# Performance work log

Hardware: AMD Instinct MI355X
Metric: run time of the kernel (lower is better)

## Reference

```python
import jax, jax.numpy as jnp
import numpy as np

EMBED = 1024
HEADS = 16
HDIM = 64
OUT = 1024
SCALE = HDIM ** (-0.5)


def setup_inputs() -> dict:
    key = jax.random.key(0)
    ks = jax.random.split(key, 12)
    B, L = 4, 1024
    k = jax.random.normal(ks[0], (B, L, EMBED), dtype=jnp.float32)
    q = jax.random.normal(ks[1], (B, L, EMBED), dtype=jnp.float32)
    v = jax.random.normal(ks[2], (B, L, EMBED), dtype=jnp.float32)
    # Linear params stored as [in, out]; scaled like torch default init
    lim = EMBED ** (-0.5)
    Wq = jax.random.uniform(ks[3], (EMBED, HEADS * HDIM), jnp.float32, -lim, lim)
    bq = jax.random.uniform(ks[4], (HEADS * HDIM,), jnp.float32, -lim, lim)
    Wk = jax.random.uniform(ks[5], (EMBED, HEADS * HDIM), jnp.float32, -lim, lim)
    Wv = jax.random.uniform(ks[6], (EMBED, HEADS * HDIM), jnp.float32, -lim, lim)
    limp = (HEADS * HDIM) ** (-0.5)
    Wp = jax.random.uniform(ks[7], (HEADS * HDIM, OUT), jnp.float32, -limp, limp)
    bp = jax.random.uniform(ks[8], (OUT,), jnp.float32, -limp, limp)
    attn_w = jax.random.uniform(ks[9], (2 * HDIM,), jnp.float32, -SCALE, SCALE)
    gamma = jnp.ones((OUT,), jnp.float32)
    beta = jnp.zeros((OUT,), jnp.float32)
    return {"k": k, "q": q, "v": v, "Wq": Wq, "bq": bq, "Wk": Wk, "Wv": Wv,
            "Wp": Wp, "bp": bp, "attn_w": attn_w, "gamma": gamma, "beta": beta}


def reference(k, q, v, Wq, bq, Wk, Wv, Wp, bp, attn_w, gamma, beta):
    B, Lq = q.shape[0], q.shape[1]
    Lk = k.shape[1]
    # QKV projections -> (b, len, heads, hdim)
    qh = (q @ Wq + bq).reshape(B, Lq, HEADS, HDIM)
    kh = (k @ Wk).reshape(B, Lk, HEADS, HDIM)
    vh = (v @ Wv).reshape(B, Lk, HEADS, HDIM)
    # mlp score: tanh(cat(q_i, k_j) . w) == tanh(q_i.w1 + k_j.w2); avoids
    # materializing the (b, q, k, n, 2d) padded tensor from the original.
    w1, w2 = attn_w[:HDIM], attn_w[HDIM:]
    sq = jnp.einsum('bind,d->bin', qh, w1)  # (b, q_len, heads)
    sk = jnp.einsum('bjnd,d->bjn', kh, w2)  # (b, k_len, heads)
    attn = jnp.tanh(sq[:, :, None, :] + sk[:, None, :, :])  # (b, i, j, n)
    attn = jax.nn.softmax(attn, axis=2)  # softmax over k_len (dim=2)
    out = jnp.einsum('bijn,bjnd->bind', attn, vh).reshape(B, Lq, HEADS * HDIM)
    out = out @ Wp + bp
    # LayerNorm eps=1e-6 (dropout is identity at p=0)
    mean = jnp.mean(out, axis=-1, keepdims=True)
    var = jnp.var(out, axis=-1, keepdims=True)
    out = (out - mean) / jnp.sqrt(var + 1e-6) * gamma + beta
    return out
```

## Files before the change

### kernel.cpp

```cpp
#include <hip/hip_runtime.h>
#include <math.h>

#define HEADS 16
#define HDIM  64
#define SEQ   1024
#define ROWS  4096
#define EMB   1024
#define MN    16

typedef _Float16 f16;
typedef __attribute__((ext_vector_type(4))) _Float16 f16x4;
typedef __attribute__((ext_vector_type(8))) _Float16 f16x8;
typedef __attribute__((ext_vector_type(4))) float f32x4;

__global__ __launch_bounds__(256) void fold_kernel(
    const float* __restrict__ Wq, const float* __restrict__ Wk,
    const float* __restrict__ bq, const float* __restrict__ attn_w,
    float* __restrict__ uq, float* __restrict__ uk, float* __restrict__ cq)
{
  int bid = blockIdx.x;
  if (bid < 128) {
    int idx = bid*256 + threadIdx.x;
    bool isQ = idx < 16384;
    int li = isQ ? idx : idx - 16384;
    int e = li >> 4, n = li & 15;
    const float* W = isQ ? Wq : Wk;
    const float* w = isQ ? attn_w : attn_w + HDIM;
    const float* wp = &W[(size_t)e*EMB + n*HDIM];
    float s = 0.f;
    #pragma unroll 16
    for (int d = 0; d < HDIM; ++d) s = fmaf(wp[d], w[d], s);
    (isQ ? uq : uk)[li] = s;
  } else if (threadIdx.x < 16) {
    int n = threadIdx.x;
    float s = 0.f;
    for (int d = 0; d < HDIM; ++d) s = fmaf(bq[n*HDIM+d], attn_w[d], s);
    cq[n] = s;
  }
}

__global__ __launch_bounds__(256) void sqsk2_kernel(
    const float* __restrict__ q, const float* __restrict__ k,
    const float* __restrict__ uq, const float* __restrict__ uk,
    const float* __restrict__ cq, float* __restrict__ sq, float* __restrict__ sk)
{
  __shared__ float rowbuf[8][EMB];
  __shared__ float part[16][8][17];
  int bid = blockIdx.x;
  bool isQ = bid < 512;
  int row0 = (isQ ? bid : bid - 512) * 8;
  const float* X = isQ ? q : k;
  const float* U = isQ ? uq : uk;
  int tid = threadIdx.x;
  #pragma unroll
  for (int p = 0; p < 8; ++p) {
    int fi = p*256 + tid;
    int r = fi >> 8, c4 = (fi & 255) * 4;
    *reinterpret_cast<float4*>(&rowbuf[r][c4]) =
        *reinterpret_cast<const float4*>(&X[(size_t)(row0 + r)*EMB + c4]);
  }
  __syncthreads();
  int n = tid & 15, ch = tid >> 4;
  float acc[8] = {0,0,0,0,0,0,0,0};
  #pragma unroll 4
  for (int e0 = 0; e0 < 64; ++e0) {
    int e = ch*64 + e0;
    float u = U[e*16 + n];
    #pragma unroll
    for (int r = 0; r < 8; ++r) acc[r] = fmaf(rowbuf[r][e], u, acc[r]);
  }
  #pragma unroll
  for (int r = 0; r < 8; ++r) part[ch][r][n] = acc[r];
  __syncthreads();
  if (tid < 128) {
    int r = tid >> 4, nn = tid & 15;
    float t = isQ ? cq[nn] : 0.f;
    #pragma unroll
    for (int c = 0; c < 16; ++c) t += part[c][r][nn];
    (isQ ? sq : sk)[(size_t)(row0 + r)*16 + nn] = t;
  }
}

__global__ __launch_bounds__(256) void nodes_kernel(const float* __restrict__ sq,
                                                    float* __restrict__ nodes)
{
  int bn = blockIdx.x;
  int b = bn >> 4, n = bn & 15;
  int tid = threadIdx.x;
  float mn = 1e30f, mx = -1e30f;
  #pragma unroll
  for (int s = 0; s < 4; ++s) {
    float v = sq[((size_t)(b*SEQ + tid + s*256))*16 + n];
    mn = fminf(mn, v); mx = fmaxf(mx, v);
  }
  __shared__ float smn[256], smx[256];
  smn[tid] = mn; smx[tid] = mx;
  __syncthreads();
  for (int off = 128; off > 0; off >>= 1) {
    if (tid < off) { smn[tid] = fminf(smn[tid], smn[tid+off]);
                     smx[tid] = fmaxf(smx[tid], smx[tid+off]); }
    __syncthreads();
  }
  if (tid < MN) {
    float c = 0.5f*(smn[0] + smx[0]);
    float r = fmaxf(0.5f*(smx[0] - smn[0]), 1e-4f);
    nodes[bn*MN + tid] = c + r * cosf(tid * (3.14159265358979323f / (MN-1)));
  }
}

__global__ __launch_bounds__(256) void ztrans_kernel(
    const float* __restrict__ v, const float* __restrict__ Wv,
    f16* __restrict__ vTh, f16* __restrict__ WvTh)
{
  __shared__ float tile[64][65];
  const int z = blockIdx.z;
  const int r0 = blockIdx.y * 64, c0 = blockIdx.x * 64;
  const int t = threadIdx.x, rr = t >> 4, c4 = (t & 15) * 4;
  const float* src = (z < 4) ? &v[(size_t)(z*SEQ + r0)*EMB + c0]
                             : &Wv[(size_t)r0*EMB + c0];
  #pragma unroll
  for (int i = 0; i < 4; ++i) {
    int row = rr + i * 16;
    float4 w = *reinterpret_cast<const float4*>(&src[(size_t)row*EMB + c4]);
    tile[row][c4] = w.x; tile[row][c4+1] = w.y;
    tile[row][c4+2] = w.z; tile[row][c4+3] = w.w;
  }
  __syncthreads();
  #pragma unroll
  for (int i = 0; i < 4; ++i) {
    int cc = rr + i * 16;
    f16x4 hh;
    #pragma unroll
    for (int jj = 0; jj < 4; ++jj) hh[jj] = (f16)tile[c4 + jj][cc];
    size_t o = (z < 4) ? ((size_t)(z*EMB + c0 + cc))*SEQ + r0 + c4
                       : ((size_t)(c0 + cc))*EMB + r0 + c4;
    *reinterpret_cast<f16x4*>(&((z < 4) ? vTh : WvTh)[o]) = hh;
  }
}

__global__ __launch_bounds__(256) void wmat_kernel(
    const float* __restrict__ sk, const float* __restrict__ nodes,
    f16* __restrict__ wh, float* __restrict__ Wn)
{
  __shared__ float sksh[256], nodesh[MN], Wnl[MN];
  const int qd = blockIdx.x, n = blockIdx.y, b = blockIdx.z;
  const int tid = threadIdx.x;
  const int j = qd*256 + tid;
  sksh[tid] = sk[((size_t)(b*SEQ + j))*16 + n];
  if (tid < MN) { nodesh[tid] = nodes[(b*16+n)*MN + tid]; Wnl[tid] = 0.f; }
  __syncthreads();
  const float skv = sksh[tid];
  const int lane = tid & 63;
  #pragma unroll 4
  for (int m = 0; m < MN; ++m) {
    float s = nodesh[m] + skv;
    float e2 = __expf(2.f * s);
    float th = 1.f - 2.f / (e2 + 1.f);
    float w = __expf(th);
    size_t row = (size_t)(b*256 + n*MN + m);
    wh[row*1024 + j] = (f16)w;
    float ws = w;
    #pragma unroll
    for (int off = 32; off > 0; off >>= 1) ws += __shfl_xor(ws, off);
    if (lane == 0) atomicAdd(&Wnl[m], ws);
  }
  __syncthreads();
  if (tid < MN) atomicAdd(&Wn[(b*16+n)*MN + tid], Wnl[tid]);
}

__global__ __launch_bounds__(256) void gemm1_f16(
    const f16* __restrict__ Ah, const f16* __restrict__ Bh,
    f16* __restrict__ Ch)
{
  __shared__ __align__(16) char lds[16384];
  const int tid = threadIdx.x;
  const int wid = tid >> 6, lane = tid & 63;
  int flat = blockIdx.y * 16 + blockIdx.x;
  int swz = (flat & 7) * 32 + (flat >> 3);
  const int bx = swz & 15, by = swz >> 4;
  const int z = by >> 2;
  const int grow = by * 64;
  const int bcol = bx * 64;
  const int wm = wid >> 1, wn = wid & 1;
  const int asel = lane >> 4, l15 = lane & 15;
  const int K = 1024, N = 1024;
  const f16* Bz_h = Bh + (size_t)z*EMB*SEQ;

  f32x4 acc[2][2];
  #pragma unroll
  for (int i = 0; i < 2; ++i)
    #pragma unroll
    for (int jx = 0; jx < 2; ++jx)
      acc[i][jx] = (f32x4){0.f, 0.f, 0.f, 0.f};

  for (int t = 0; t < 16; ++t) {
    const int k0 = t * 64;
    __syncthreads();
    #pragma unroll
    for (int r = 0; r < 4; ++r) {
      int ci = ((r & 1) << 8) + tid;
      int row = ci >> 3, kc = ci & 7;
      int kcg = kc ^ (row & 7);
      const f16* base = (r < 2) ? Ah : Bz_h;
      size_t roff = (r < 2) ? (size_t)(grow + row) : (size_t)(bcol + row);
      const char* src = (const char*)(base + roff * K + k0 + kcg * 8);
      char* dst = lds + (r * 256 + wid * 64) * 16;
      __builtin_amdgcn_global_load_lds(
          (const __attribute__((address_space(1))) unsigned int*)src,
          (__attribute__((address_space(3))) unsigned int*)dst, 16, 0, 0);
    }
    __syncthreads();
    #pragma unroll
    for (int kk = 0; kk < 2; ++kk) {
      f16x8 afh[2], bfh[2];
      #pragma unroll
      for (int mf = 0; mf < 2; ++mf) {
        int row = wm * 32 + mf * 16 + l15;
        int kcx = (kk * 4 + asel) ^ (row & 7);
        afh[mf] = *reinterpret_cast<const f16x8*>(lds + row * 128 + kcx * 16);
      }
      #pragma unroll
      for (int nf = 0; nf < 2; ++nf) {
        int col = wn * 32 + nf * 16 + l15;
        int kcx = (kk * 4 + asel) ^ (col & 7);
        bfh[nf] = *reinterpret_cast<const f16x8*>(lds + 8192 + col * 128 + kcx * 16);
      }
      #pragma unroll
      for (int mf = 0; mf < 2; ++mf)
        #pragma unroll
        for (int nf = 0; nf < 2; ++nf)
          acc[mf][nf] = __builtin_amdgcn_mfma_f32_16x16x32_f16(afh[mf], bfh[nf], acc[mf][nf], 0, 0, 0);
    }
  }
  const int crow0 = grow + wm * 32 + asel * 4;
  const int ccol0 = bcol + wn * 32 + l15;
  #pragma unroll
  for (int nf = 0; nf < 2; ++nf)
    #pragma unroll
    for (int mf = 0; mf < 2; ++mf)
      #pragma unroll
      for (int jx = 0; jx < 4; ++jx)
        Ch[(size_t)(crow0 + mf*16 + jx) * N + ccol0 + nf*16] = (f16)acc[mf][nf][jx];
}

__global__ __launch_bounds__(256) void coeff2_kernel(
    const float* __restrict__ sq, const float* __restrict__ nodes,
    const float* __restrict__ Wn, f16* __restrict__ csh, f16* __restrict__ csl)
{
  __shared__ float nsh[16][MN], wsh[16][MN];
  const int ic = blockIdx.x, b = blockIdx.y;
  const int tid = threadIdx.x;
  {
    int nn = tid >> 4, mm = tid & 15;
    nsh[nn][mm] = nodes[(b*16+nn)*MN + mm];
    wsh[nn][mm] = Wn[(b*16+nn)*MN + mm];
  }
  __syncthreads();
  const int il = tid >> 4, n = tid & 15;
  const int i = ic*16 + il;
  float s = sq[((size_t)(b*SEQ + i))*16 + n];
  float lam[MN];
  float den = 0.f;
  int ex = -1;
  #pragma unroll
  for (int m = 0; m < MN; ++m) {
    float diff = s - nsh[n][m];
    float wb = ((m == 0) | (m == MN-1)) ? 0.5f : 1.0f;
    wb = (m & 1) ? -wb : wb;
    if (diff == 0.f) ex = m;
    lam[m] = wb / diff;
    den = fmaf(lam[m], wsh[n][m], den);
  }
  float rden = 1024.f / den;
  f16* hp = &csh[((size_t)(b*SEQ + i))*256 + n*MN];
  f16* lp = &csl[((size_t)(b*SEQ + i))*256 + n*MN];
  #pragma unroll
  for (int m8 = 0; m8 < 2; ++m8) {
    f16x8 hv, lv;
    #pragma unroll
    for (int jj = 0; jj < 8; ++jj) {
      int m = m8*8 + jj;
      float c = (ex >= 0) ? ((m == ex) ? 1024.f/wsh[n][ex] : 0.f) : lam[m]*rden;
      f16 h = (f16)c;
      hv[jj] = h; lv[jj] = (f16)(c - (float)h);
    }
    *reinterpret_cast<f16x8*>(&hp[m8*8]) = hv;
    *reinterpret_cast<f16x8*>(&lp[m8*8]) = lv;
  }
}

__global__ __launch_bounds__(256) void ghprep_kernel(
    const f16* __restrict__ Ph, const f16* __restrict__ WvTh,
    const float* __restrict__ Wp, f16* __restrict__ Hsh, f16* __restrict__ Hsl)
{
  __shared__ float Gsh[MN][64];
  const int oc = blockIdx.x, n = blockIdx.y, b = blockIdx.z;
  const int bn = b*16 + n;
  const int tid = threadIdx.x;
  const int w = tid >> 6, lane = tid & 63;
  const int l15 = lane & 15, asel = lane >> 4;
  f32x4 acc = (f32x4){0.f,0.f,0.f,0.f};
  #pragma unroll 4
  for (int ks = 0; ks < 32; ++ks) {
    size_t bo = ((size_t)(n*64 + w*16 + l15))*1024 + ks*32 + asel*8;
    f16x8 bh = *reinterpret_cast<const f16x8*>(&WvTh[bo]);
    size_t ao = ((size_t)(bn*MN + l15))*1024 + ks*32 + asel*8;
    f16x8 ah = *reinterpret_cast<const f16x8*>(&Ph[ao]);
    acc = __builtin_amdgcn_mfma_f32_16x16x32_f16(ah, bh, acc, 0, 0, 0);
  }
  #pragma unroll
  for (int jx = 0; jx < 4; ++jx)
    Gsh[asel*4 + jx][w*16 + l15] = acc[jx];
  __syncthreads();
  const int o = oc*256 + tid;
  float a2[MN];
  #pragma unroll
  for (int m = 0; m < MN; ++m) a2[m] = 0.f;
  for (int d = 0; d < 64; ++d) {
    float wp = Wp[(size_t)(n*64 + d)*1024 + o];
    #pragma unroll
    for (int m = 0; m < MN; ++m) a2[m] = fmaf(wp, Gsh[m][d], a2[m]);
  }
  f16 hbuf[MN], lbuf[MN];
  #pragma unroll
  for (int m = 0; m < MN; ++m) {
    float vv = a2[m] * (1.f/1024.f);
    f16 h = (f16)vv;
    hbuf[m] = h; lbuf[m] = (f16)(vv - (float)h);
  }
  size_t base = ((size_t)(b*1024 + o))*256 + n*MN;
  #pragma unroll
  for (int m8 = 0; m8 < 2; ++m8) {
    *reinterpret_cast<f16x8*>(&Hsh[base + m8*8]) = *reinterpret_cast<f16x8*>(&hbuf[m8*8]);
    *reinterpret_cast<f16x8*>(&Hsl[base + m8*8]) = *reinterpret_cast<f16x8*>(&lbuf[m8*8]);
  }
}

__global__ __launch_bounds__(256) void gemm2_k(
    const f16* __restrict__ Ah, const f16* __restrict__ Al,
    const f16* __restrict__ Bh, const f16* __restrict__ Bl,
    const float* __restrict__ bias, float* __restrict__ Cf)
{
  __shared__ __align__(16) char lds[49152];
  const int tid = threadIdx.x;
  const int wid = tid >> 6, lane = tid & 63;
  int flat = (blockIdx.z * 8 + blockIdx.y) * 16 + blockIdx.x;
  int swz = (flat & 7) * 64 + (flat >> 3);
  const int bx = swz & 15;
  const int t2 = swz >> 4;
  const int by = t2 & 7, z = t2 >> 3;
  const int brow = by * 128;
  const int bcol = bx * 64;
  const int wm = wid >> 1, wn = wid & 1;
  const int asel = lane >> 4, l15 = lane & 15;
  const int K = 256, N = 1024, MZ = 1024;
  const f16* Az_h = Ah + (size_t)z*MZ*K;
  const f16* Az_l = Al + (size_t)z*MZ*K;
  const f16* Bz_h = Bh + (size_t)z*N*K;
  const f16* Bz_l = Bl + (size_t)z*N*K;

  f32x4 acc[4][2];
  #pragma unroll
  for (int i = 0; i < 4; ++i)
    #pragma unroll
    for (int jx = 0; jx < 2; ++jx)
      acc[i][jx] = (f32x4){0.f, 0.f, 0.f, 0.f};

  for (int t = 0; t < 4; ++t) {
    const int k0 = t * 64;
    __syncthreads();
    #pragma unroll
    for (int r = 0; r < 12; ++r) {
      const char* src;
      if (r < 8) {
        int ci = ((r & 3) << 8) + tid;
        int row = ci >> 3, kc = ci & 7;
        int kcg = kc ^ (row & 7);
        const f16* base = (r < 4) ? Az_h : Az_l;
        src = (const char*)(base + (size_t)(brow + row) * K + k0 + kcg * 8);
      } else {
        int ci = ((r & 1) << 8) + tid;
        int col = ci >> 3, kc = ci & 7;
        int kcg = kc ^ (col & 7);
        const f16* base = (r < 10) ? Bz_h : Bz_l;
        src = (const char*)(base + (size_t)(bcol + col) * K + k0 + kcg * 8);
      }
      char* dst = lds + (r * 256 + wid * 64) * 16;
      __builtin_amdgcn_global_load_lds(
          (const __attribute__((address_space(1))) unsigned int*)src,
          (__attribute__((address_space(3))) unsigned int*)dst, 16, 0, 0);
    }
    __syncthreads();
    #pragma unroll
    for (int kk = 0; kk < 2; ++kk) {
      f16x8 afh[4], afl[4], bfh[2], bfl[2];
      #pragma unroll
      for (int mf = 0; mf < 4; ++mf) {
        int row = wm * 64 + mf * 16 + l15;
        int kcx = (kk * 4 + asel) ^ (row & 7);
        int off = row * 128 + kcx * 16;
        afh[mf] = *reinterpret_cast<const f16x8*>(lds + off);
        afl[mf] = *reinterpret_cast<const f16x8*>(lds + 16384 + off);
      }
      #pragma unroll
      for (int nf = 0; nf < 2; ++nf) {
        int col = wn * 32 + nf * 16 + l15;
        int kcx = (kk * 4 + asel) ^ (col & 7);
        int off = col * 128 + kcx * 16;
        bfh[nf] = *reinterpret_cast<const f16x8*>(lds + 32768 + off);
        bfl[nf] = *reinterpret_cast<const f16x8*>(lds + 40960 + off);
      }
      #pragma unroll
      for (int mf = 0; mf < 4; ++mf)
        #pragma unroll
        for (int nf = 0; nf < 2; ++nf) {
          acc[mf][nf] = __builtin_amdgcn_mfma_f32_16x16x32_f16(afh[mf], bfh[nf], acc[mf][nf], 0, 0, 0);
          acc[mf][nf] = __builtin_amdgcn_mfma_f32_16x16x32_f16(afh[mf], bfl[nf], acc[mf][nf], 0, 0, 0);
          acc[mf][nf] = __builtin_amdgcn_mfma_f32_16x16x32_f16(afl[mf], bfh[nf], acc[mf][nf], 0, 0, 0);
        }
    }
  }
  const int crow0 = z*MZ + brow + wm * 64 + asel * 4;
  const int ccol0 = bcol + wn * 32 + l15;
  #pragma unroll
  for (int nf = 0; nf < 2; ++nf) {
    float bv = bias[ccol0 + nf * 16];
    #pragma unroll
    for (int mf = 0; mf < 4; ++mf)
      #pragma unroll
      for (int jx = 0; jx < 4; ++jx)
        Cf[(size_t)(crow0 + mf*16 + jx) * N + ccol0 + nf*16] = acc[mf][nf][jx] + bv;
  }
}

__global__ __launch_bounds__(256) void ln_kernel(
    float* __restrict__ out, const float* __restrict__ gamma,
    const float* __restrict__ beta)
{
  int row = blockIdx.x, tid = threadIdx.x;
  float4 x = *reinterpret_cast<float4*>(&out[(size_t)row*EMB + tid*4]);
  float sum = x.x + x.y + x.z + x.w;
  float ssq = x.x*x.x + x.y*x.y + x.z*x.z + x.w*x.w;
  #pragma unroll
  for (int off = 32; off > 0; off >>= 1) {
    sum += __shfl_down(sum, off);
    ssq += __shfl_down(ssq, off);
  }
  __shared__ float red[8];
  int wave = tid >> 6, lane = tid & 63;
  if (lane == 0) { red[wave] = sum; red[4+wave] = ssq; }
  __syncthreads();
  if (tid == 0) {
    float a = red[0]+red[1]+red[2]+red[3];
    float qq = red[4]+red[5]+red[6]+red[7];
    float mean = a * (1.f/EMB);
    float var  = qq * (1.f/EMB) - mean*mean;
    red[0] = mean;
    red[1] = 1.0f / sqrtf(var + 1e-6f);
  }
  __syncthreads();
  float mean = red[0], inv = red[1];
  float4 gv = *reinterpret_cast<const float4*>(&gamma[tid*4]);
  float4 bv = *reinterpret_cast<const float4*>(&beta[tid*4]);
  x.x = (x.x - mean)*inv*gv.x + bv.x;
  x.y = (x.y - mean)*inv*gv.y + bv.y;
  x.z = (x.z - mean)*inv*gv.z + bv.z;
  x.w = (x.w - mean)*inv*gv.w + bv.w;
  *reinterpret_cast<float4*>(&out[(size_t)row*EMB + tid*4]) = x;
}

extern "C" void kernel_launch(void* const* d_in, const int* in_sizes, int n_in,
                              void* d_out, int out_size, void* d_ws, size_t ws_size,
                              hipStream_t stream)
{
  const float* k   = (const float*)d_in[0];
  const float* q   = (const float*)d_in[1];
  const float* v   = (const float*)d_in[2];
  const float* Wq  = (const float*)d_in[3];
  const float* bq  = (const float*)d_in[4];
  const float* Wk  = (const float*)d_in[5];
  const float* Wv  = (const float*)d_in[6];
  const float* Wp  = (const float*)d_in[7];
  const float* bp  = (const float*)d_in[8];
  const float* aw  = (const float*)d_in[9];
  const float* gamma = (const float*)d_in[10];
  const float* beta  = (const float*)d_in[11];
  float* out = (float*)d_out;

  float* ws    = (float*)d_ws;
  float* uq    = ws;
  float* uk    = uq + 16384;
  float* cq    = uk + 16384;
  float* sq    = cq + 16;
  float* sk    = sq + 65536;
  float* nodes = sk + 65536;
  float* Wn    = nodes + 1024;
  const size_t MEG = 1048576;
  f16* f16b  = (f16*)(ws + 165904);
  f16* WvTh  = f16b;
  f16* vTh   = f16b + 1*MEG;
  f16* wh    = f16b + 5*MEG;
  f16* Ph    = f16b + 6*MEG;
  f16* csh   = f16b + 7*MEG;
  f16* csl   = f16b + 8*MEG;
  f16* Hsh   = f16b + 9*MEG;
  f16* Hsl   = f16b + 10*MEG;

  fold_kernel<<<129, 256, 0, stream>>>(Wq, Wk, bq, aw, uq, uk, cq);
  sqsk2_kernel<<<1024, 256, 0, stream>>>(q, k, uq, uk, cq, sq, sk);
  nodes_kernel<<<64, 256, 0, stream>>>(sq, nodes);
  ztrans_kernel<<<dim3(16,16,5), 256, 0, stream>>>(v, Wv, vTh, WvTh);
  hipMemsetAsync(Wn, 0, 1024*sizeof(float), stream);
  wmat_kernel<<<dim3(4,16,4), 256, 0, stream>>>(sk, nodes, wh, Wn);
  gemm1_f16<<<dim3(16,16), 256, 0, stream>>>(wh, vTh, Ph);
  coeff2_kernel<<<dim3(64,4), 256, 0, stream>>>(sq, nodes, Wn, csh, csl);
  ghprep_kernel<<<dim3(4,16,4), 256, 0, stream>>>(Ph, WvTh, Wp, Hsh, Hsl);
  gemm2_k<<<dim3(16,8,4), 256, 0, stream>>>(csh, csl, Hsh, Hsl, bp, out);
  ln_kernel<<<ROWS, 256, 0, stream>>>(out, gamma, beta);
}
```

Measured before the change: 196.1 us.

## Fuse all stages into one persistent cooperative kernel with grid syncs

```diff
diff --git a/kernel.cpp b/kernel.cpp
--- a/kernel.cpp
+++ b/kernel.cpp
@@ -1,10 +1,10 @@
 #include <hip/hip_runtime.h>
+#include <hip/hip_cooperative_groups.h>
 #include <math.h>
 
-#define HEADS 16
-#define HDIM  64
+namespace cg = cooperative_groups;
+
 #define SEQ   1024
-#define ROWS  4096
 #define EMB   1024
 #define MN    16
 
@@ -13,508 +13,479 @@
 typedef __attribute__((ext_vector_type(8))) _Float16 f16x8;
 typedef __attribute__((ext_vector_type(4))) float f32x4;
 
-__global__ __launch_bounds__(256) void fold_kernel(
-    const float* __restrict__ Wq, const float* __restrict__ Wk,
-    const float* __restrict__ bq, const float* __restrict__ attn_w,
-    float* __restrict__ uq, float* __restrict__ uk, float* __restrict__ cq)
+struct Params {
+  const float *k, *q, *v, *Wq, *bq, *Wk, *Wv, *Wp, *bp, *aw, *gamma, *beta;
+  float *out;
+  float *uq, *uk, *cq, *sq, *sk, *nodes, *Wn;
+  f16 *WvTh, *vTh, *wh, *Ph, *csh, *csl, *Hsh, *Hsl;
+  int NB;
+};
+
+__global__ __launch_bounds__(256, 4) void mega_kernel(Params P)
 {
-  int bid = blockIdx.x;
-  if (bid < 128) {
-    int idx = bid*256 + threadIdx.x;
-    bool isQ = idx < 16384;
-    int li = isQ ? idx : idx - 16384;
-    int e = li >> 4, n = li & 15;
-    const float* W = isQ ? Wq : Wk;
-    const float* w = isQ ? attn_w : attn_w + HDIM;
-    const float* wp = &W[(size_t)e*EMB + n*HDIM];
-    float s = 0.f;
-    #pragma unroll 16
-    for (int d = 0; d < HDIM; ++d) s = fmaf(wp[d], w[d], s);
-    (isQ ? uq : uk)[li] = s;
-  } else if (threadIdx.x < 16) {
-    int n = threadIdx.x;
-    float s = 0.f;
-    for (int d = 0; d < HDIM; ++d) s = fmaf(bq[n*HDIM+d], attn_w[d], s);
-    cq[n] = s;
-  }
-}
-
-__global__ __launch_bounds__(256) void sqsk2_kernel(
-    const float* __restrict__ q, const float* __restrict__ k,
-    const float* __restrict__ uq, const float* __restrict__ uk,
-    const float* __restrict__ cq, float* __restrict__ sq, float* __restrict__ sk)
-{
-  __shared__ float rowbuf[8][EMB];
-  __shared__ float part[16][8][17];
-  int bid = blockIdx.x;
-  bool isQ = bid < 512;
-  int row0 = (isQ ? bid : bid - 512) * 8;
-  const float* X = isQ ? q : k;
-  const float* U = isQ ? uq : uk;
-  int tid = threadIdx.x;
-  #pragma unroll
-  for (int p = 0; p < 8; ++p) {
-    int fi = p*256 + tid;
-    int r = fi >> 8, c4 = (fi & 255) * 4;
-    *reinterpret_cast<float4*>(&rowbuf[r][c4]) =
-        *reinterpret_cast<const float4*>(&X[(size_t)(row0 + r)*EMB + c4]);
-  }
-  __syncthreads();
-  int n = tid & 15, ch = tid >> 4;
-  float acc[8] = {0,0,0,0,0,0,0,0};
-  #pragma unroll 4
-  for (int e0 = 0; e0 < 64; ++e0) {
-    int e = ch*64 + e0;
-    float u = U[e*16 + n];
-    #pragma unroll
-    for (int r = 0; r < 8; ++r) acc[r] = fmaf(rowbuf[r][e], u, acc[r]);
-  }
-  #pragma unroll
-  for (int r = 0; r < 8; ++r) part[ch][r][n] = acc[r];
-  __syncthreads();
-  if (tid < 128) {
-    int r = tid >> 4, nn = tid & 15;
-    float t = isQ ? cq[nn] : 0.f;
-    #pragma unroll
-    for (int c = 0; c < 16; ++c) t += part[c][r][nn];
-    (isQ ? sq : sk)[(size_t)(row0 + r)*16 + nn] = t;
-  }
-}
-
-__global__ __launch_bounds__(256) void nodes_kernel(const float* __restrict__ sq,
-                                                    float* __restrict__ nodes)
-{
-  int bn = blockIdx.x;
-  int b = bn >> 4, n = bn & 15;
-  int tid = threadIdx.x;
-  float mn = 1e30f, mx = -1e30f;
-  #pragma unroll
-  for (int s = 0; s < 4; ++s) {
-    float v = sq[((size_t)(b*SEQ + tid + s*256))*16 + n];
-    mn = fminf(mn, v); mx = fmaxf(mx, v);
-  }
-  __shared__ float smn[256], smx[256];
-  smn[tid] = mn; smx[tid] = mx;
-  __syncthreads();
-  for (int off = 128; off > 0; off >>= 1) {
-    if (tid < off) { smn[tid] = fminf(smn[tid], smn[tid+off]);
-                     smx[tid] = fmaxf(smx[tid], smx[tid+off]); }
-    __syncthreads();
-  }
-  if (tid < MN) {
-    float c = 0.5f*(smn[0] + smx[0]);
-    float r = fmaxf(0.5f*(smx[0] - smn[0]), 1e-4f);
-    nodes[bn*MN + tid] = c + r * cosf(tid * (3.14159265358979323f / (MN-1)));
-  }
-}
-
-__global__ __launch_bounds__(256) void ztrans_kernel(
-    const float* __restrict__ v, const float* __restrict__ Wv,
-    f16* __restrict__ vTh, f16* __restrict__ WvTh)
-{
-  __shared__ float tile[64][65];
-  const int z = blockIdx.z;
-  const int r0 = blockIdx.y * 64, c0 = blockIdx.x * 64;
-  const int t = threadIdx.x, rr = t >> 4, c4 = (t & 15) * 4;
-  const float* src = (z < 4) ? &v[(size_t)(z*SEQ + r0)*EMB + c0]
-                             : &Wv[(size_t)r0*EMB + c0];
-  #pragma unroll
-  for (int i = 0; i < 4; ++i) {
-    int row = rr + i * 16;
-    float4 w = *reinterpret_cast<const float4*>(&src[(size_t)row*EMB + c4]);
-    tile[row][c4] = w.x; tile[row][c4+1] = w.y;
-    tile[row][c4+2] = w.z; tile[row][c4+3] = w.w;
-  }
-  __syncthreads();
-  #pragma unroll
-  for (int i = 0; i < 4; ++i) {
-    int cc = rr + i * 16;
-    f16x4 hh;
-    #pragma unroll
-    for (int jj = 0; jj < 4; ++jj) hh[jj] = (f16)tile[c4 + jj][cc];
-    size_t o = (z < 4) ? ((size_t)(z*EMB + c0 + cc))*SEQ + r0 + c4
-                       : ((size_t)(c0 + cc))*EMB + r0 + c4;
-    *reinterpret_cast<f16x4*>(&((z < 4) ? vTh : WvTh)[o]) = hh;
-  }
-}
-
-__global__ __launch_bounds__(256) void wmat_kernel(
-    const float* __restrict__ sk, const float* __restrict__ nodes,
-    f16* __restrict__ wh, float* __restrict__ Wn)
-{
-  __shared__ float sksh[256], nodesh[MN], Wnl[MN];
-  const int qd = blockIdx.x, n = blockIdx.y, b = blockIdx.z;
-  const int tid = threadIdx.x;
-  const int j = qd*256 + tid;
-  sksh[tid] = sk[((size_t)(b*SEQ + j))*16 + n];
-  if (tid < MN) { nodesh[tid] = nodes[(b*16+n)*MN + tid]; Wnl[tid] = 0.f; }
-  __syncthreads();
-  const float skv = sksh[tid];
-  const int lane = tid & 63;
-  #pragma unroll 4
-  for (int m = 0; m < MN; ++m) {
-    float s = nodesh[m] + skv;
-    float e2 = __expf(2.f * s);
-    float th = 1.f - 2.f / (e2 + 1.f);
-    float w = __expf(th);
-    size_t row = (size_t)(b*256 + n*MN + m);
-    wh[row*1024 + j] = (f16)w;
-    float ws = w;
-    #pragma unroll
-    for (int off = 32; off > 0; off >>= 1) ws += __shfl_xor(ws, off);
-    if (lane == 0) atomicAdd(&Wnl[m], ws);
-  }
-  __syncthreads();
-  if (tid < MN) atomicAdd(&Wn[(b*16+n)*MN + tid], Wnl[tid]);
-}
-
-__global__ __launch_bounds__(256) void gemm1_f16(
-    const f16* __restrict__ Ah, const f16* __restrict__ Bh,
-    f16* __restrict__ Ch)
-{
-  __shared__ __align__(16) char lds[16384];
-  const int tid = threadIdx.x;
-  const int wid = tid >> 6, lane = tid & 63;
-  int flat = blockIdx.y * 16 + blockIdx.x;
-  int swz = (flat & 7) * 32 + (flat >> 3);
-  const int bx = swz & 15, by = swz >> 4;
-  const int z = by >> 2;
-  const int grow = by * 64;
-  const int bcol = bx * 64;
-  const int wm = wid >> 1, wn = wid & 1;
-  const int asel = lane >> 4, l15 = lane & 15;
-  const int K = 1024, N = 1024;
-  const f16* Bz_h = Bh + (size_t)z*EMB*SEQ;
-
-  f32x4 acc[2][2];
-  #pragma unroll
-  for (int i = 0; i < 2; ++i)
-    #pragma unroll
-    for (int jx = 0; jx < 2; ++jx)
-      acc[i][jx] = (f32x4){0.f, 0.f, 0.f, 0.f};
-
-  for (int t = 0; t < 16; ++t) {
-    const int k0 = t * 64;
-    __syncthreads();
-    #pragma unroll
-    for (int r = 0; r < 4; ++r) {
-      int ci = ((r & 1) << 8) + tid;
-      int row = ci >> 3, kc = ci & 7;
-      int kcg = kc ^ (row & 7);
-      const f16* base = (r < 2) ? Ah : Bz_h;
-      size_t roff = (r < 2) ? (size_t)(grow + row) : (size_t)(bcol + row);
-      const char* src = (const char*)(base + roff * K + k0 + kcg * 8);
-      char* dst = lds + (r * 256 + wid * 64) * 16;
-      __builtin_amdgcn_global_load_lds(
-          (const __attribute__((address_space(1))) unsigned int*)src,
-          (__attribute__((address_space(3))) unsigned int*)dst, 16, 0, 0);
-    }
-    __syncthreads();
-    #pragma unroll
-    for (int kk = 0; kk < 2; ++kk) {
-      f16x8 afh[2], bfh[2];
-      #pragma unroll
-      for (int mf = 0; mf < 2; ++mf) {
-        int row = wm * 32 + mf * 16 + l15;
-        int kcx = (kk * 4 + asel) ^ (row & 7);
-        afh[mf] = *reinterpret_cast<const f16x8*>(lds + row * 128 + kcx * 16);
-      }
-      #pragma unroll
-      for (int nf = 0; nf < 2; ++nf) {
-        int col = wn * 32 + nf * 16 + l15;
-        int kcx = (kk * 4 + asel) ^ (col & 7);
-        bfh[nf] = *reinterpret_cast<const f16x8*>(lds + 8192 + col * 128 + kcx * 16);
-      }
-      #pragma unroll
-      for (int mf = 0; mf < 2; ++mf)
-        #pragma unroll
-        for (int nf = 0; nf < 2; ++nf)
-          acc[mf][nf] = __builtin_amdgcn_mfma_f32_16x16x32_f16(afh[mf], bfh[nf], acc[mf][nf], 0, 0, 0);
-    }
-  }
-  const int crow0 = grow + wm * 32 + asel * 4;
-  const int ccol0 = bcol + wn * 32 + l15;
-  #pragma unroll
-  for (int nf = 0; nf < 2; ++nf)
-    #pragma unroll
-    for (int mf = 0; mf < 2; ++mf)
-      #pragma unroll
-      for (int jx = 0; jx < 4; ++jx)
-        Ch[(size_t)(crow0 + mf*16 + jx) * N + ccol0 + nf*16] = (f16)acc[mf][nf][jx];
-}
-
-__global__ __launch_bounds__(256) void coeff2_kernel(
-    const float* __restrict__ sq, const float* __restrict__ nodes,
-    const float* __restrict__ Wn, f16* __restrict__ csh, f16* __restrict__ csl)
-{
-  __shared__ float nsh[16][MN], wsh[16][MN];
-  const int ic = blockIdx.x, b = blockIdx.y;
-  const int tid = threadIdx.x;
-  {
-    int nn = tid >> 4, mm = tid & 15;
-    nsh[nn][mm] = nodes[(b*16+nn)*MN + mm];
-    wsh[nn][mm] = Wn[(b*16+nn)*MN + mm];
-  }
-  __syncthreads();
-  const int il = tid >> 4, n = tid & 15;
-  const int i = ic*16 + il;
-  float s = sq[((size_t)(b*SEQ + i))*16 + n];
-  float lam[MN];
-  float den = 0.f;
-  int ex = -1;
-  #pragma unroll
-  for (int m = 0; m < MN; ++m) {
-    float diff = s - nsh[n][m];
-    float wb = ((m == 0) | (m == MN-1)) ? 0.5f : 1.0f;
-    wb = (m & 1) ? -wb : wb;
-    if (diff == 0.f) ex = m;
-    lam[m] = wb / diff;
-    den = fmaf(lam[m], wsh[n][m], den);
-  }
-  float rden = 1024.f / den;
-  f16* hp = &csh[((size_t)(b*SEQ + i))*256 + n*MN];
-  f16* lp = &csl[((size_t)(b*SEQ + i))*256 + n*MN];
-  #pragma unroll
-  for (int m8 = 0; m8 < 2; ++m8) {
-    f16x8 hv, lv;
-    #pragma unroll
-    for (int jj = 0; jj < 8; ++jj) {
-      int m = m8*8 + jj;
-      float c = (ex >= 0) ? ((m == ex) ? 1024.f/wsh[n][ex] : 0.f) : lam[m]*rden;
-      f16 h = (f16)c;
-      hv[jj] = h; lv[jj] = (f16)(c - (float)h);
-    }
-    *reinterpret_cast<f16x8*>(&hp[m8*8]) = hv;
-    *reinterpret_cast<f16x8*>(&lp[m8*8]) = lv;
-  }
-}
-
-__global__ __launch_bounds__(256) void ghprep_kernel(
-    const f16* __restrict__ Ph, const f16* __restrict__ WvTh,
-    const float* __restrict__ Wp, f16* __restrict__ Hsh, f16* __restrict__ Hsl)
-{
-  __shared__ float Gsh[MN][64];
-  const int oc = blockIdx.x, n = blockIdx.y, b = blockIdx.z;
-  const int bn = b*16 + n;
-  const int tid = threadIdx.x;
-  const int w = tid >> 6, lane = tid & 63;
-  const int l15 = lane & 15, asel = lane >> 4;
-  f32x4 acc = (f32x4){0.f,0.f,0.f,0.f};
-  #pragma unroll 4
-  for (int ks = 0; ks < 32; ++ks) {
-    size_t bo = ((size_t)(n*64 + w*16 + l15))*1024 + ks*32 + asel*8;
-    f16x8 bh = *reinterpret_cast<const f16x8*>(&WvTh[bo]);
-    size_t ao = ((size_t)(bn*MN + l15))*1024 + ks*32 + asel*8;
-    f16x8 ah = *reinterpret_cast<const f16x8*>(&Ph[ao]);
-    acc = __builtin_amdgcn_mfma_f32_16x16x32_f16(ah, bh, acc, 0, 0, 0);
-  }
-  #pragma unroll
-  for (int jx = 0; jx < 4; ++jx)
-    Gsh[asel*4 + jx][w*16 + l15] = acc[jx];
-  __syncthreads();
-  const int o = oc*256 + tid;
-  float a2[MN];
-  #pragma unroll
-  for (int m = 0; m < MN; ++m) a2[m] = 0.f;
-  for (int d = 0; d < 64; ++d) {
-    float wp = Wp[(size_t)(n*64 + d)*1024 + o];
-    #pragma unroll
-    for (int m = 0; m < MN; ++m) a2[m] = fmaf(wp, Gsh[m][d], a2[m]);
-  }
-  f16 hbuf[MN], lbuf[MN];
-  #pragma unroll
-  for (int m = 0; m < MN; ++m) {
-    float vv = a2[m] * (1.f/1024.f);
-    f16 h = (f16)vv;
-    hbuf[m] = h; lbuf[m] = (f16)(vv - (float)h);
-  }
-  size_t base = ((size_t)(b*1024 + o))*256 + n*MN;
-  #pragma unroll
-  for (int m8 = 0; m8 < 2; ++m8) {
-    *reinterpret_cast<f16x8*>(&Hsh[base + m8*8]) = *reinterpret_cast<f16x8*>(&hbuf[m8*8]);
-    *reinterpret_cast<f16x8*>(&Hsl[base + m8*8]) = *reinterpret_cast<f16x8*>(&lbuf[m8*8]);
-  }
-}
-
-__global__ __launch_bounds__(256) void gemm2_k(
-    const f16* __restrict__ Ah, const f16* __restrict__ Al,
-    const f16* __restrict__ Bh, const f16* __restrict__ Bl,
-    const float* __restrict__ bias, float* __restrict__ Cf)
-{
-  __shared__ __align__(16) char lds[49152];
-  const int tid = threadIdx.x;
-  const int wid = tid >> 6, lane = tid & 63;
-  int flat = (blockIdx.z * 8 + blockIdx.y) * 16 + blockIdx.x;
-  int swz = (flat & 7) * 64 + (flat >> 3);
-  const int bx = swz & 15;
-  const int t2 = swz >> 4;
-  const int by = t2 & 7, z = t2 >> 3;
-  const int brow = by * 128;
-  const int bcol = bx * 64;
-  const int wm = wid >> 1, wn = wid & 1;
-  const int asel = lane >> 4, l15 = lane & 15;
-  const int K = 256, N = 1024, MZ = 1024;
-  const f16* Az_h = Ah + (size_t)z*MZ*K;
-  const f16* Az_l = Al + (size_t)z*MZ*K;
-  const f16* Bz_h = Bh + (size_t)z*N*K;
-  const f16* Bz_l = Bl + (size_t)z*N*K;
-
-  f32x4 acc[4][2];
-  #pragma unroll
-  for (int i = 0; i < 4; ++i)
-    #pragma unroll
-    for (int jx = 0; jx < 2; ++jx)
-      acc[i][jx] = (f32x4){0.f, 0.f, 0.f, 0.f};
-
-  for (int t = 0; t < 4; ++t) {
-    const int k0 = t * 64;
-    __syncthreads();
-    #pragma unroll
-    for (int r = 0; r < 12; ++r) {
-      const char* src;
-      if (r < 8) {
-        int ci = ((r & 3) << 8) + tid;
+  __shared__ __align__(16) char SMEM[36864];
+  cg::grid_group grid = cg::this_grid();
+  const int bid = blockIdx.x, tid = threadIdx.x;
+  const int NB = P.NB;
+
+  for (int t = bid; t < 1410; t += NB) {
+    __syncthreads();
+    if (t < 128) {
+      int idx = t*256 + tid;
+      bool isQ = idx < 16384;
+      int li = isQ ? idx : idx - 16384;
+      int e = li >> 4, n = li & 15;
+      const float* W = isQ ? P.Wq : P.Wk;
+      const float* w = isQ ? P.aw : P.aw + 64;
+      const float* wp = &W[(size_t)e*EMB + n*64];
+      float s = 0.f;
+      #pragma unroll 16
+      for (int d = 0; d < 64; ++d) s = fmaf(wp[d], w[d], s);
+      (isQ ? P.uq : P.uk)[li] = s;
+    } else if (t < 1408) {
+      int tt = t - 128;
+      int z = tt >> 8;
+      int ty = (tt >> 4) & 15, tx = tt & 15;
+      float (*tile)[65] = (float(*)[65])SMEM;
+      int r0 = ty*64, c0 = tx*64;
+      const float* src = (z < 4) ? &P.v[(size_t)(z*SEQ + r0)*EMB + c0]
+                                 : &P.Wv[(size_t)r0*EMB + c0];
+      int rr = tid >> 4, c4 = (tid & 15)*4;
+      #pragma unroll
+      for (int i = 0; i < 4; ++i) {
+        int row = rr + i*16;
+        float4 wv = *reinterpret_cast<const float4*>(&src[(size_t)row*EMB + c4]);
+        tile[row][c4] = wv.x; tile[row][c4+1] = wv.y;
+        tile[row][c4+2] = wv.z; tile[row][c4+3] = wv.w;
+      }
+      __syncthreads();
+      #pragma unroll
+      for (int i = 0; i < 4; ++i) {
+        int cc = rr + i*16;
+        f16x4 hh;
+        #pragma unroll
+        for (int jj = 0; jj < 4; ++jj) hh[jj] = (f16)tile[c4+jj][cc];
+        size_t o = (z < 4) ? ((size_t)(z*EMB + c0 + cc))*SEQ + r0 + c4
+                           : ((size_t)(c0 + cc))*EMB + r0 + c4;
+        *reinterpret_cast<f16x4*>(&((z < 4) ? P.vTh : P.WvTh)[o]) = hh;
+      }
+    } else if (t == 1408) {
+      if (tid < 16) {
+        float s = 0.f;
+        for (int d = 0; d < 64; ++d) s = fmaf(P.bq[tid*64+d], P.aw[d], s);
+        P.cq[tid] = s;
+      }
+    } else {
+      for (int u = tid; u < 1024; u += 256) P.Wn[u] = 0.f;
+    }
+  }
+  grid.sync();
+
+  for (int t = bid; t < 1024; t += NB) {
+    bool isQ = t < 512;
+    int row0 = (isQ ? t : t - 512)*8;
+    const float* X = isQ ? P.q : P.k;
+    const float* U = isQ ? P.uq : P.uk;
+    float (*rowbuf)[1024] = (float(*)[1024])SMEM;
+    __syncthreads();
+    #pragma unroll
+    for (int p = 0; p < 8; ++p) {
+      int fi = p*256 + tid;
+      int r = fi >> 8, c4 = (fi & 255)*4;
+      *reinterpret_cast<float4*>(&rowbuf[r][c4]) =
+          *reinterpret_cast<const float4*>(&X[(size_t)(row0+r)*EMB + c4]);
+    }
+    __syncthreads();
+    int n = tid & 15, ch = tid >> 4;
+    float acc[8] = {0,0,0,0,0,0,0,0};
+    #pragma unroll 4
+    for (int e0 = 0; e0 < 64; ++e0) {
+      int e = ch*64 + e0;
+      float u = U[e*16 + n];
+      #pragma unroll
+      for (int r = 0; r < 8; ++r) acc[r] = fmaf(rowbuf[r][e], u, acc[r]);
+    }
+    __syncthreads();
+    float (*part)[8][17] = (float(*)[8][17])SMEM;
+    #pragma unroll
+    for (int r = 0; r < 8; ++r) part[ch][r][n] = acc[r];
+    __syncthreads();
+    if (tid < 128) {
+      int r = tid >> 4, nn = tid & 15;
+      float s = isQ ? P.cq[nn] : 0.f;
+      #pragma unroll
+      for (int c = 0; c < 16; ++c) s += part[c][r][nn];
+      (isQ ? P.sq : P.sk)[(size_t)(row0+r)*16 + nn] = s;
+    }
+  }
+  grid.sync();
+
+  for (int t = bid; t < 64; t += NB) {
+    int b = t >> 4, n = t & 15;
+    float mn = 1e30f, mx = -1e30f;
+    #pragma unroll
+    for (int s = 0; s < 4; ++s) {
+      float vv = P.sq[((size_t)(b*SEQ + tid + s*256))*16 + n];
+      mn = fminf(mn, vv); mx = fmaxf(mx, vv);
+    }
+    float* smn = (float*)SMEM;
+    float* smx = smn + 256;
+    __syncthreads();
+    smn[tid] = mn; smx[tid] = mx;
+    __syncthreads();
+    for (int off = 128; off > 0; off >>= 1) {
+      if (tid < off) { smn[tid] = fminf(smn[tid], smn[tid+off]);
+                       smx[tid] = fmaxf(smx[tid], smx[tid+off]); }
+      __syncthreads();
+    }
+    if (tid < MN) {
+      float c = 0.5f*(smn[0]+smx[0]);
+      float r = fmaxf(0.5f*(smx[0]-smn[0]), 1e-4f);
+      P.nodes[t*MN + tid] = c + r*cosf(tid*(3.14159265358979323f/(MN-1)));
+    }
+  }
+  grid.sync();
+
+  for (int t = bid; t < 1024; t += NB) {
+    int b = t >> 8, n = (t >> 4) & 15, qd = t & 15;
+    int j0 = qd*64;
+    float* nodesh = (float*)SMEM;
+    __syncthreads();
+    if (tid < MN) nodesh[tid] = P.nodes[(b*16+n)*MN + tid];
+    __syncthreads();
+    int jl = tid & 63, mg = tid >> 6;
+    int j = j0 + jl;
+    float skv = P.sk[((size_t)(b*SEQ + j))*16 + n];
+    #pragma unroll
+    for (int mm = 0; mm < 4; ++mm) {
+      int m = mg*4 + mm;
+      float s = nodesh[m] + skv;
+      float e2 = __expf(2.f*s);
+      float th = 1.f - 2.f/(e2+1.f);
+      float w = __expf(th);
+      P.wh[(size_t)(b*256 + n*MN + m)*1024 + j] = (f16)w;
+      float ws = w;
+      #pragma unroll
+      for (int off = 32; off > 0; off >>= 1) ws += __shfl_xor(ws, off);
+      if (jl == 0) atomicAdd(&P.Wn[(b*16+n)*MN + m], ws);
+    }
+  }
+  grid.sync();
+
+  for (int t = bid; t < 512; t += NB) {
+    __syncthreads();
+    if (t < 256) {
+      int swz = (t & 7)*32 + (t >> 3);
+      int bx = swz & 15, by = swz >> 4;
+      int z = by >> 2;
+      int grow = by*64, bcol = bx*64;
+      int wid = tid >> 6, lane = tid & 63;
+      int wm = wid >> 1, wn = wid & 1;
+      int asel = lane >> 4, l15 = lane & 15;
+      const f16* Bz = P.vTh + (size_t)z*EMB*SEQ;
+      char* lds = SMEM;
+      f32x4 acc[2][2];
+      #pragma unroll
+      for (int i = 0; i < 2; ++i)
+        #pragma unroll
+        for (int jx = 0; jx < 2; ++jx)
+          acc[i][jx] = (f32x4){0.f,0.f,0.f,0.f};
+      for (int kt = 0; kt < 16; ++kt) {
+        const int k0 = kt*64;
+        __syncthreads();
+        #pragma unroll
+        for (int r = 0; r < 4; ++r) {
+          int ci = ((r & 1) << 8) + tid;
+          int row = ci >> 3, kc = ci & 7;
+          int kcg = kc ^ (row & 7);
+          const f16* base = (r < 2) ? P.wh : Bz;
+          size_t roff = (r < 2) ? (size_t)(grow + row) : (size_t)(bcol + row);
+          const char* src = (const char*)(base + roff*1024 + k0 + kcg*8);
+          char* dst = lds + (r*256 + wid*64)*16;
+          __builtin_amdgcn_global_load_lds(
+              (const __attribute__((address_space(1))) unsigned int*)src,
+              (__attribute__((address_space(3))) unsigned int*)dst, 16, 0, 0);
+        }
+        __syncthreads();
+        #pragma unroll
+        for (int kk = 0; kk < 2; ++kk) {
+          f16x8 afh[2], bfh[2];
+          #pragma unroll
+          for (int mf = 0; mf < 2; ++mf) {
+            int row = wm*32 + mf*16 + l15;
+            int kcx = (kk*4 + asel) ^ (row & 7);
+            afh[mf] = *reinterpret_cast<const f16x8*>(lds + row*128 + kcx*16);
+          }
+          #pragma unroll
+          for (int nf = 0; nf < 2; ++nf) {
+            int col = wn*32 + nf*16 + l15;
+            int kcx = (kk*4 + asel) ^ (col & 7);
+            bfh[nf] = *reinterpret_cast<const f16x8*>(lds + 8192 + col*128 + kcx*16);
+          }
+          #pragma unroll
+          for (int mf = 0; mf < 2; ++mf)
+            #pragma unroll
+            for (int nf = 0; nf < 2; ++nf)
+              acc[mf][nf] = __builtin_amdgcn_mfma_f32_16x16x32_f16(afh[mf], bfh[nf], acc[mf][nf], 0, 0, 0);
+        }
+      }
+      const int crow0 = grow + wm*32 + asel*4;
+      const int ccol0 = bcol + wn*32 + l15;
+      #pragma unroll
+      for (int nf = 0; nf < 2; ++nf)
+        #pragma unroll
+        for (int mf = 0; mf < 2; ++mf)
+          #pragma unroll
+          for (int jx = 0; jx < 4; ++jx)
+            P.Ph[(size_t)(crow0 + mf*16 + jx)*1024 + ccol0 + nf*16] = (f16)acc[mf][nf][jx];
+    } else {
+      int tc = t - 256;
+      int ic = tc & 63, b = tc >> 6;
+      float (*nsh)[MN] = (float(*)[MN])SMEM;
+      float (*wsh)[MN] = ((float(*)[MN])SMEM) + 16;
+      {
+        int nn = tid >> 4, mm = tid & 15;
+        nsh[nn][mm] = P.nodes[(b*16+nn)*MN + mm];
+        wsh[nn][mm] = P.Wn[(b*16+nn)*MN + mm];
+      }
+      __syncthreads();
+      int il = tid >> 4, n = tid & 15;
+      int i = ic*16 + il;
+      float s = P.sq[((size_t)(b*SEQ + i))*16 + n];
+      float lam[MN];
+      float den = 0.f;
+      int ex = -1;
+      #pragma unroll
+      for (int m = 0; m < MN; ++m) {
+        float diff = s - nsh[n][m];
+        float wb = ((m == 0) | (m == MN-1)) ? 0.5f : 1.0f;
+        wb = (m & 1) ? -wb : wb;
+        if (diff == 0.f) ex = m;
+        lam[m] = wb / diff;
+        den = fmaf(lam[m], wsh[n][m], den);
+      }
+      float rden = 1024.f / den;
+      f16* hp = &P.csh[((size_t)(b*SEQ + i))*256 + n*MN];
+      f16* lp = &P.csl[((size_t)(b*SEQ + i))*256 + n*MN];
+      #pragma unroll
+      for (int m8 = 0; m8 < 2; ++m8) {
+        f16x8 hv, lv;
+        #pragma unroll
+        for (int jj = 0; jj < 8; ++jj) {
+          int m = m8*8 + jj;
+          float c = (ex >= 0) ? ((m == ex) ? 1024.f/wsh[n][ex] : 0.f) : lam[m]*rden;
+          f16 h = (f16)c;
+          hv[jj] = h; lv[jj] = (f16)(c - (float)h);
+        }
+        *reinterpret_cast<f16x8*>(&hp[m8*8]) = hv;
+        *reinterpret_cast<f16x8*>(&lp[m8*8]) = lv;
+      }
+    }
+  }
+  grid.sync();
+
+  for (int t = bid; t < 256; t += NB) {
+    int oc = t & 3, n = (t >> 2) & 15, b = t >> 6;
+    int bn = b*16 + n;
+    float (*Gsh)[64] = (float(*)[64])SMEM;
+    int w = tid >> 6, lane = tid & 63;
+    int l15 = lane & 15, asel = lane >> 4;
+    __syncthreads();
+    f32x4 acc = (f32x4){0.f,0.f,0.f,0.f};
+    #pragma unroll 4
+    for (int ks = 0; ks < 32; ++ks) {
+      size_t bo = ((size_t)(n*64 + w*16 + l15))*1024 + ks*32 + asel*8;
+      f16x8 bh = *reinterpret_cast<const f16x8*>(&P.WvTh[bo]);
+      size_t ao = ((size_t)(bn*MN + l15))*1024 + ks*32 + asel*8;
+      f16x8 ah = *reinterpret_cast<const f16x8*>(&P.Ph[ao]);
+      acc = __builtin_amdgcn_mfma_f32_16x16x32_f16(ah, bh, acc, 0, 0, 0);
+    }
+    #pragma unroll
+    for (int jx = 0; jx < 4; ++jx)
+      Gsh[asel*4 + jx][w*16 + l15] = acc[jx];
+    __syncthreads();
+    int o = oc*256 + tid;
+    float a2[MN];
+    #pragma unroll
+    for (int m = 0; m < MN; ++m) a2[m] = 0.f;
+    for (int d = 0; d < 64; ++d) {
+      float wp = P.Wp[(size_t)(n*64 + d)*1024 + o];
+      #pragma unroll
+      for (int m = 0; m < MN; ++m) a2[m] = fmaf(wp, Gsh[m][d], a2[m]);
+    }
+    f16 hbuf[MN], lbuf[MN];
+    #pragma unroll
+    for (int m = 0; m < MN; ++m) {
+      float vv = a2[m] * (1.f/1024.f);
+      f16 h = (f16)vv;
+      hbuf[m] = h; lbuf[m] = (f16)(vv - (float)h);
+    }
+    size_t base = ((size_t)(b*1024 + o))*256 + n*MN;
+    #pragma unroll
+    for (int m8 = 0; m8 < 2; ++m8) {
+      *reinterpret_cast<f16x8*>(&P.Hsh[base + m8*8]) = *reinterpret_cast<f16x8*>(&hbuf[m8*8]);
+      *reinterpret_cast<f16x8*>(&P.Hsl[base + m8*8]) = *reinterpret_cast<f16x8*>(&lbuf[m8*8]);
+    }
+  }
+  grid.sync();
+
+  for (int t = bid; t < 1024; t += NB) {
+    int swz = (t & 7)*128 + (t >> 3);
+    int bx = swz & 15;
+    int by = swz >> 4;
+    int row0 = by*64;
+    int bcol = bx*64;
+    int z = by >> 4;
+    const f16* Bzh = P.Hsh + (size_t)z*1024*256;
+    const f16* Bzl = P.Hsl + (size_t)z*1024*256;
+    int wid = tid >> 6, lane = tid & 63;
+    int wm = wid >> 1, wn = wid & 1;
+    int asel = lane >> 4, l15 = lane & 15;
+    char* lds = SMEM;
+    f32x4 acc[2][2];
+    #pragma unroll
+    for (int i = 0; i < 2; ++i)
+      #pragma unroll
+      for (int jx = 0; jx < 2; ++jx)
+        acc[i][jx] = (f32x4){0.f,0.f,0.f,0.f};
+    for (int kt = 0; kt < 4; ++kt) {
+      const int k0 = kt*64;
+      __syncthreads();
+      #pragma unroll
+      for (int r = 0; r < 8; ++r) {
+        int ci = ((r & 1) << 8) + tid;
         int row = ci >> 3, kc = ci & 7;
         int kcg = kc ^ (row & 7);
-        const f16* base = (r < 4) ? Az_h : Az_l;
-        src = (const char*)(base + (size_t)(brow + row) * K + k0 + kcg * 8);
-      } else {
-        int ci = ((r & 1) << 8) + tid;
-        int col = ci >> 3, kc = ci & 7;
-        int kcg = kc ^ (col & 7);
-        const f16* base = (r < 10) ? Bz_h : Bz_l;
-        src = (const char*)(base + (size_t)(bcol + col) * K + k0 + kcg * 8);
-      }
-      char* dst = lds + (r * 256 + wid * 64) * 16;
-      __builtin_amdgcn_global_load_lds(
-          (const __attribute__((address_space(1))) unsigned int*)src,
-          (__attribute__((address_space(3))) unsigned int*)dst, 16, 0, 0);
-    }
-    __syncthreads();
-    #pragma unroll
-    for (int kk = 0; kk < 2; ++kk) {
-      f16x8 afh[4], afl[4], bfh[2], bfl[2];
-      #pragma unroll
-      for (int mf = 0; mf < 4; ++mf) {
-        int row = wm * 64 + mf * 16 + l15;
-        int kcx = (kk * 4 + asel) ^ (row & 7);
-        int off = row * 128 + kcx * 16;
-        afh[mf] = *reinterpret_cast<const f16x8*>(lds + off);
-        afl[mf] = *reinterpret_cast<const f16x8*>(lds + 16384 + off);
-      }
-      #pragma unroll
-      for (int nf = 0; nf < 2; ++nf) {
-        int col = wn * 32 + nf * 16 + l15;
-        int kcx = (kk * 4 + asel) ^ (col & 7);
-        int off = col * 128 + kcx * 16;
-        bfh[nf] = *reinterpret_cast<const f16x8*>(lds + 32768 + off);
-        bfl[nf] = *reinterpret_cast<const f16x8*>(lds + 40960 + off);
-      }
-      #pragma unroll
-      for (int mf = 0; mf < 4; ++mf)
+        const f16* base = (r < 2) ? P.csh : (r < 4) ? P.csl : (r < 6) ? Bzh : Bzl;
+        size_t roff = (r < 4) ? (size_t)(row0 + row)*256 : (size_t)(bcol + row)*256;
+        const char* src = (const char*)(base + roff + k0 + kcg*8);
+        char* dst = lds + (r*256 + wid*64)*16;
+        __builtin_amdgcn_global_load_lds(
+            (const __attribute__((address_space(1))) unsigned int*)src,
+            (__attribute__((address_space(3))) unsigned int*)dst, 16, 0, 0);
+      }
+      __syncthreads();
+      #pragma unroll
+      for (int kk = 0; kk < 2; ++kk) {
+        f16x8 afh[2], afl[2], bfh[2], bfl[2];
+        #pragma unroll
+        for (int mf = 0; mf < 2; ++mf) {
+          int row = wm*32 + mf*16 + l15;
+          int kcx = (kk*4 + asel) ^ (row & 7);
+          afh[mf] = *reinterpret_cast<const f16x8*>(lds + row*128 + kcx*16);
+          afl[mf] = *reinterpret_cast<const f16x8*>(lds + 8192 + row*128 + kcx*16);
+        }
         #pragma unroll
         for (int nf = 0; nf < 2; ++nf) {
-          acc[mf][nf] = __builtin_amdgcn_mfma_f32_16x16x32_f16(afh[mf], bfh[nf], acc[mf][nf], 0, 0, 0);
-          acc[mf][nf] = __builtin_amdgcn_mfma_f32_16x16x32_f16(afh[mf], bfl[nf], acc[mf][nf], 0, 0, 0);
-          acc[mf][nf] = __builtin_amdgcn_mfma_f32_16x16x32_f16(afl[mf], bfh[nf], acc[mf][nf], 0, 0, 0);
+          int col = wn*32 + nf*16 + l15;
+          int kcx = (kk*4 + asel) ^ (col & 7);
+          bfh[nf] = *reinterpret_cast<const f16x8*>(lds + 16384 + col*128 + kcx*16);
+          bfl[nf] = *reinterpret_cast<const f16x8*>(lds + 24576 + col*128 + kcx*16);
         }
-    }
-  }
-  const int crow0 = z*MZ + brow + wm * 64 + asel * 4;
-  const int ccol0 = bcol + wn * 32 + l15;
-  #pragma unroll
-  for (int nf = 0; nf < 2; ++nf) {
-    float bv = bias[ccol0 + nf * 16];
-    #pragma unroll
-    for (int mf = 0; mf < 4; ++mf)
-      #pragma unroll
-      for (int jx = 0; jx < 4; ++jx)
-        Cf[(size_t)(crow0 + mf*16 + jx) * N + ccol0 + nf*16] = acc[mf][nf][jx] + bv;
-  }
-}
-
-__global__ __launch_bounds__(256) void ln_kernel(
-    float* __restrict__ out, const float* __restrict__ gamma,
-    const float* __restrict__ beta)
-{
-  int row = blockIdx.x, tid = threadIdx.x;
-  float4 x = *reinterpret_cast<float4*>(&out[(size_t)row*EMB + tid*4]);
-  float sum = x.x + x.y + x.z + x.w;
-  float ssq = x.x*x.x + x.y*x.y + x.z*x.z + x.w*x.w;
-  #pragma unroll
-  for (int off = 32; off > 0; off >>= 1) {
-    sum += __shfl_down(sum, off);
-    ssq += __shfl_down(ssq, off);
-  }
-  __shared__ float red[8];
-  int wave = tid >> 6, lane = tid & 63;
-  if (lane == 0) { red[wave] = sum; red[4+wave] = ssq; }
-  __syncthreads();
-  if (tid == 0) {
-    float a = red[0]+red[1]+red[2]+red[3];
-    float qq = red[4]+red[5]+red[6]+red[7];
-    float mean = a * (1.f/EMB);
-    float var  = qq * (1.f/EMB) - mean*mean;
-    red[0] = mean;
-    red[1] = 1.0f / sqrtf(var + 1e-6f);
-  }
-  __syncthreads();
-  float mean = red[0], inv = red[1];
-  float4 gv = *reinterpret_cast<const float4*>(&gamma[tid*4]);
-  float4 bv = *reinterpret_cast<const float4*>(&beta[tid*4]);
-  x.x = (x.x - mean)*inv*gv.x + bv.x;
-  x.y = (x.y - mean)*inv*gv.y + bv.y;
-  x.z = (x.z - mean)*inv*gv.z + bv.z;
-  x.w = (x.w - mean)*inv*gv.w + bv.w;
-  *reinterpret_cast<float4*>(&out[(size_t)row*EMB + tid*4]) = x;
+        #pragma unroll
+        for (int mf = 0; mf < 2; ++mf)
+          #pragma unroll
+          for (int nf = 0; nf < 2; ++nf) {
+            acc[mf][nf] = __builtin_amdgcn_mfma_f32_16x16x32_f16(afh[mf], bfh[nf], acc[mf][nf], 0, 0, 0);
+            acc[mf][nf] = __builtin_amdgcn_mfma_f32_16x16x32_f16(afh[mf], bfl[nf], acc[mf][nf], 0, 0, 0);
+            acc[mf][nf] = __builtin_amdgcn_mfma_f32_16x16x32_f16(afl[mf], bfh[nf], acc[mf][nf], 0, 0, 0);
+          }
+      }
+    }
+    const int crow0 = row0 + wm*32 + asel*4;
+    const int ccol0 = bcol + wn*32 + l15;
+    #pragma unroll
+    for (int nf = 0; nf < 2; ++nf) {
+      float bv = P.bp[ccol0 + nf*16];
+      #pragma unroll
+      for (int mf = 0; mf < 2; ++mf)
+        #pragma unroll
+        for (int jx = 0; jx < 4; ++jx)
+          P.out[(size_t)(crow0 + mf*16 + jx)*1024 + ccol0 + nf*16] = acc[mf][nf][jx] + bv;
+    }
+  }
+  grid.sync();
+
+  for (int t = bid; t < 1024; t += NB) {
+    int wid = tid >> 6, lane = tid & 63;
+    int row = t*4 + wid;
+    float4 x[4];
+    float sum = 0.f, ssq = 0.f;
+    #pragma unroll
+    for (int p = 0; p < 4; ++p) {
+      x[p] = *reinterpret_cast<float4*>(&P.out[(size_t)row*1024 + (p*64 + lane)*4]);
+      sum += x[p].x + x[p].y + x[p].z + x[p].w;
+      ssq += x[p].x*x[p].x + x[p].y*x[p].y + x[p].z*x[p].z + x[p].w*x[p].w;
+    }
+    #pragma unroll
+    for (int off = 32; off > 0; off >>= 1) {
+      sum += __shfl_xor(sum, off);
+      ssq += __shfl_xor(ssq, off);
+    }
+    float mean = sum * (1.f/1024.f);
+    float var  = ssq * (1.f/1024.f) - mean*mean;
+    float inv  = 1.0f / sqrtf(var + 1e-6f);
+    #pragma unroll
+    for (int p = 0; p < 4; ++p) {
+      float4 gv = *reinterpret_cast<const float4*>(&P.gamma[(p*64 + lane)*4]);
+      float4 bv = *reinterpret_cast<const float4*>(&P.beta[(p*64 + lane)*4]);
+      float4 y;
+      y.x = (x[p].x - mean)*inv*gv.x + bv.x;
+      y.y = (x[p].y - mean)*inv*gv.y + bv.y;
+      y.z = (x[p].z - mean)*inv*gv.z + bv.z;
+      y.w = (x[p].w - mean)*inv*gv.w + bv.w;
+      *reinterpret_cast<float4*>(&P.out[(size_t)row*1024 + (p*64 + lane)*4]) = y;
+    }
+  }
 }
 
 extern "C" void kernel_launch(void* const* d_in, const int* in_sizes, int n_in,
                               void* d_out, int out_size, void* d_ws, size_t ws_size,
                               hipStream_t stream)
 {
-  const float* k   = (const float*)d_in[0];
-  const float* q   = (const float*)d_in[1];
-  const float* v   = (const float*)d_in[2];
-  const float* Wq  = (const float*)d_in[3];
-  const float* bq  = (const float*)d_in[4];
-  const float* Wk  = (const float*)d_in[5];
-  const float* Wv  = (const float*)d_in[6];
-  const float* Wp  = (const float*)d_in[7];
-  const float* bp  = (const float*)d_in[8];
-  const float* aw  = (const float*)d_in[9];
-  const float* gamma = (const float*)d_in[10];
-  const float* beta  = (const float*)d_in[11];
-  float* out = (float*)d_out;
-
-  float* ws    = (float*)d_ws;
-  float* uq    = ws;
-  float* uk    = uq + 16384;
-  float* cq    = uk + 16384;
-  float* sq    = cq + 16;
-  float* sk    = sq + 65536;
-  float* nodes = sk + 65536;
-  float* Wn    = nodes + 1024;
+  Params prm;
+  prm.k   = (const float*)d_in[0];
+  prm.q   = (const float*)d_in[1];
+  prm.v   = (const float*)d_in[2];
+  prm.Wq  = (const float*)d_in[3];
+  prm.bq  = (const float*)d_in[4];
+  prm.Wk  = (const float*)d_in[5];
+  prm.Wv  = (const float*)d_in[6];
+  prm.Wp  = (const float*)d_in[7];
+  prm.bp  = (const float*)d_in[8];
+  prm.aw  = (const float*)d_in[9];
+  prm.gamma = (const float*)d_in[10];
+  prm.beta  = (const float*)d_in[11];
+  prm.out = (float*)d_out;
+
+  float* ws = (float*)d_ws;
+  prm.uq    = ws;
+  prm.uk    = prm.uq + 16384;
+  prm.cq    = prm.uk + 16384;
+  prm.sq    = prm.cq + 16;
+  prm.sk    = prm.sq + 65536;
+  prm.nodes = prm.sk + 65536;
+  prm.Wn    = prm.nodes + 1024;
   const size_t MEG = 1048576;
-  f16* f16b  = (f16*)(ws + 165904);
-  f16* WvTh  = f16b;
-  f16* vTh   = f16b + 1*MEG;
-  f16* wh    = f16b + 5*MEG;
-  f16* Ph    = f16b + 6*MEG;
-  f16* csh   = f16b + 7*MEG;
-  f16* csl   = f16b + 8*MEG;
-  f16* Hsh   = f16b + 9*MEG;
-  f16* Hsl   = f16b + 10*MEG;
-
-  fold_kernel<<<129, 256, 0, stream>>>(Wq, Wk, bq, aw, uq, uk, cq);
-  sqsk2_kernel<<<1024, 256, 0, stream>>>(q, k, uq, uk, cq, sq, sk);
-  nodes_kernel<<<64, 256, 0, stream>>>(sq, nodes);
-  ztrans_kernel<<<dim3(16,16,5), 256, 0, stream>>>(v, Wv, vTh, WvTh);
-  hipMemsetAsync(Wn, 0, 1024*sizeof(float), stream);
-  wmat_kernel<<<dim3(4,16,4), 256, 0, stream>>>(sk, nodes, wh, Wn);
-  gemm1_f16<<<dim3(16,16), 256, 0, stream>>>(wh, vTh, Ph);
-  coeff2_kernel<<<dim3(64,4), 256, 0, stream>>>(sq, nodes, Wn, csh, csl);
-  ghprep_kernel<<<dim3(4,16,4), 256, 0, stream>>>(Ph, WvTh, Wp, Hsh, Hsl);
-  gemm2_k<<<dim3(16,8,4), 256, 0, stream>>>(csh, csl, Hsh, Hsl, bp, out);
-  ln_kernel<<<ROWS, 256, 0, stream>>>(out, gamma, beta);
+  f16* f16b = (f16*)(ws + 165904);
+  prm.WvTh = f16b;
+  prm.vTh  = f16b + 1*MEG;
+  prm.wh   = f16b + 5*MEG;
+  prm.Ph   = f16b + 6*MEG;
+  prm.csh  = f16b + 7*MEG;
+  prm.csl  = f16b + 8*MEG;
+  prm.Hsh  = f16b + 9*MEG;
+  prm.Hsl  = f16b + 10*MEG;
+
+  int occ = 0;
+  hipOccupancyMaxActiveBlocksPerMultiprocessor(&occ,
+      reinterpret_cast<const void*>(mega_kernel), 256, 0);
+  if (occ < 1) occ = 1;
+  int NB = occ * 256;
+  if (NB > 1024) NB = 1024;
+  prm.NB = NB;
+
+  void* args[] = { &prm };
+  hipLaunchCooperativeKernel(reinterpret_cast<void*>(mega_kernel),
+                             dim3(NB), dim3(256), args, 0, stream);
 }
```

After: 613.0 us. 3.13x slower.
